# Kernel tuning notes

Hardware: AMD Instinct MI355X
Metric: run time of the kernel (lower is better)

The kernel has to match this reference:

```python
import jax, jax.numpy as jnp
import numpy as np

H = 64          # hidden_dim
TF = 24         # forecast_length


def _a_norm(N):
    # Complete graph (all i!=j) + GCNConv default self-loops => A+I = ones(N,N).
    # deg_i = N, so D^-1/2 (A+I) D^-1/2 = ones / N. Built generically below.
    A = jnp.ones((N, N), dtype=jnp.float32)
    deg = A.sum(axis=1)
    return A / jnp.sqrt(deg[:, None] * deg[None, :])


def _gcn(x, A, W, b):
    # PyG GCNConv: aggregate(norm * (x W)) + bias
    return jnp.einsum('ij,...jh->...ih', A, x @ W) + b


def setup_inputs() -> dict:
    key = jax.random.key(0)
    ks = jax.random.split(key, 20)
    B, N, T = 32, 128, 96
    s = lambda k, shape, fan: (jax.random.normal(k, shape, jnp.float32) / np.sqrt(max(fan, 1)))
    return {
        'x': jax.random.normal(ks[0], (B, N, T), jnp.float32),
        # spatial GCN stack
        'W_s1': s(ks[1], (1, H), 1), 'b_s1': jnp.zeros((H,), jnp.float32),
        'W_s2': s(ks[2], (H, H), H), 'b_s2': jnp.zeros((H,), jnp.float32),
        # temporal attention MLP
        'Wa1': s(ks[3], (H, H), H), 'ba1': jnp.zeros((H,), jnp.float32),
        'Wa2': s(ks[4], (H, 1), H), 'ba2': jnp.zeros((1,), jnp.float32),
        # GRU (single step, h0 = 0)
        'W_ih': s(ks[5], (3 * H, H), H), 'W_hh': s(ks[6], (3 * H, H), H),
        'b_ih': jnp.zeros((3 * H,), jnp.float32), 'b_hh': jnp.zeros((3 * H,), jnp.float32),
        # ODE-func GCN stack
        'W_o1': s(ks[7], (H, H), H), 'b_o1': jnp.zeros((H,), jnp.float32),
        'W_o2': s(ks[8], (H, H), H), 'b_o2': jnp.zeros((H,), jnp.float32),
        # output head
        'W_out': s(ks[9], (H, 1), H), 'b_out': jnp.zeros((1,), jnp.float32),
    }


def reference(x, W_s1, b_s1, W_s2, b_s2, Wa1, ba1, Wa2, ba2,
              W_ih, W_hh, b_ih, b_hh, W_o1, b_o1, W_o2, b_o2, W_out, b_out):
    B, N, T = x.shape
    A = _a_norm(N)

    # --- spatial encoding, vectorized over (batch, time) ---
    xt = jnp.transpose(x, (0, 2, 1))[..., None]          # (B, T, N, 1)
    h = jax.nn.relu(_gcn(xt, A, W_s1, b_s1))             # (B, T, N, H)
    h = jax.nn.relu(_gcn(h, A, W_s2, b_s2))

    # --- temporal attention over time axis ---
    att = jnp.tanh(h @ Wa1 + ba1) @ Wa2 + ba2            # (B, T, N, 1)
    w = jax.nn.softmax(att, axis=1)
    nf = jnp.sum(h * w, axis=1)                          # (B, N, H)

    # --- one-step GRU encoder with zero initial hidden ---
    gi = nf.reshape(B * N, -1) @ W_ih.T + b_ih           # (B*N, 3H)
    gi_r, gi_z, gi_n = jnp.split(gi, 3, axis=-1)
    bh_r, bh_z, bh_n = jnp.split(b_hh, 3)
    r = jax.nn.sigmoid(gi_r + bh_r)
    z = jax.nn.sigmoid(gi_z + bh_z)
    n = jnp.tanh(gi_n + r * bh_n)
    hidden = ((1.0 - z) * n).reshape(B, N, -1)           # (B, N, H)

    # --- graph ODE derivative: two GCN layers + tanh ---
    def f(y):
        y = jnp.tanh(_gcn(y, A, W_o1, b_o1))
        y = jnp.tanh(_gcn(y, A, W_o2, b_o2))
        return y

    # torchdiffeq fixed-grid 'rk4' (3/8 rule) on t = linspace(0, TF, TF)
    dt = jnp.float32(TF / (TF - 1))
    third = jnp.float32(1.0 / 3.0)

    def step(y, _):
        k1 = f(y)
        k2 = f(y + dt * k1 * third)
        k3 = f(y + dt * (k2 - k1 * third))
        k4 = f(y + dt * (k1 - k2 + k3))
        y1 = y + dt * (k1 + 3.0 * (k2 + k3) + k4) * jnp.float32(0.125)
        return y1, y1

    _, ys = jax.lax.scan(step, hidden, None, length=TF - 1)
    traj = jnp.concatenate([hidden[None], ys], axis=0)   # (TF, B, N, H)

    # output head then rearrange to (B, N, TF)
    preds = (traj @ W_out + b_out)[..., 0]               # (TF, B, N)
    return jnp.transpose(preds, (1, 2, 0))
```

## Files before the change

kernel.cpp:

```cpp
#include <hip/hip_runtime.h>


#define BN 32
#define NN 128
#define TT 96
#define HH 64
#define TFC 24

#if defined(__has_builtin)
#if __has_builtin(__builtin_amdgcn_fdot2)
#define HAVE_FDOT2 1
#endif
#if __has_builtin(__builtin_amdgcn_update_dpp)
#define HAVE_DPP 1
#endif
#endif

using half2v = __fp16 __attribute__((ext_vector_type(2)));
typedef _Float16 half8 __attribute__((ext_vector_type(8)));
typedef float f32x4 __attribute__((ext_vector_type(4)));

__device__ __forceinline__ unsigned pack_pair(float a, float b) {
    union { half2v h; unsigned u; } c;
    c.h = __builtin_amdgcn_cvt_pkrtz(a, b);
    return c.u;
}
__device__ __forceinline__ half2v as_h2(unsigned u) {
    union { unsigned u; half2v h; } c; c.u = u; return c.h;
}
__device__ __forceinline__ unsigned rdlu(unsigned v, int l) {
    return (unsigned)__builtin_amdgcn_readlane((int)v, l);
}
__device__ __forceinline__ float rdl(float v, int l) {
    return __int_as_float(__builtin_amdgcn_readlane(__float_as_int(v), l));
}

template <int CTRL>
__device__ __forceinline__ float dppf(float x) {
#if HAVE_DPP
    return __int_as_float(
        __builtin_amdgcn_update_dpp(0, __float_as_int(x), CTRL, 0xF, 0xF, true));
#else
    return 0.f;
#endif
}

__device__ __forceinline__ float xor1(float x) {
#if HAVE_DPP
    return dppf<0xB1>(x);
#else
    return __shfl_xor(x, 1, 64);
#endif
}

__device__ __forceinline__ float wave_sum(float v) {
#if HAVE_DPP
    v += dppf<0xB1>(v);
    v += dppf<0x4E>(v);
    v += dppf<0x141>(v);
    v += dppf<0x140>(v);
    return ((rdl(v, 0) + rdl(v, 16)) + (rdl(v, 32) + rdl(v, 48)));
#else
#pragma unroll
    for (int off = 32; off > 0; off >>= 1) v += __shfl_xor(v, off, 64);
    return v;
#endif
}
__device__ __forceinline__ void wave_sum2(float& a, float& b) {
#if HAVE_DPP
    a += dppf<0xB1>(a);  b += dppf<0xB1>(b);
    a += dppf<0x4E>(a);  b += dppf<0x4E>(b);
    a += dppf<0x141>(a); b += dppf<0x141>(b);
    a += dppf<0x140>(a); b += dppf<0x140>(b);
    a = (rdl(a, 0) + rdl(a, 16)) + (rdl(a, 32) + rdl(a, 48));
    b = (rdl(b, 0) + rdl(b, 16)) + (rdl(b, 32) + rdl(b, 48));
#else
    a = wave_sum(a); b = wave_sum(b);
#endif
}
__device__ __forceinline__ float wave_max(float v) {
#if HAVE_DPP
    v = fmaxf(v, dppf<0xB1>(v));
    v = fmaxf(v, dppf<0x4E>(v));
    v = fmaxf(v, dppf<0x141>(v));
    v = fmaxf(v, dppf<0x140>(v));
    return fmaxf(fmaxf(rdl(v, 0), rdl(v, 16)), fmaxf(rdl(v, 32), rdl(v, 48)));
#else
#pragma unroll
    for (int off = 32; off > 0; off >>= 1) v = fmaxf(v, __shfl_xor(v, off, 64));
    return v;
#endif
}

__device__ __forceinline__ float dot2acc(unsigned w, unsigned up, float acc) {
#if HAVE_FDOT2
    return __builtin_amdgcn_fdot2(as_h2(w), as_h2(up), acc, false);
#else
    const half2v wh = as_h2(w), uh = as_h2(up);
    return fmaf((float)wh.y, (float)uh.y, fmaf((float)wh.x, (float)uh.x, acc));
#endif
}

#define PMV64_2(WP, UA, UB, RA, RB)                                        \
    do {                                                                   \
        float a0 = 0.f, a1 = 0.f, a2 = 0.f, a3 = 0.f;                      \
        float b0 = 0.f, b1 = 0.f, b2 = 0.f, b3 = 0.f;                      \
        _Pragma("unroll")                                                  \
        for (int k = 0; k < 32; k += 4) {                                  \
            const unsigned ua0 = rdlu(UA, 2 * k);                          \
            const unsigned ub0 = rdlu(UB, 2 * k);                          \
            const unsigned ua1 = rdlu(UA, 2 * k + 2);                      \
            const unsigned ub1 = rdlu(UB, 2 * k + 2);                      \
            const unsigned ua2 = rdlu(UA, 2 * k + 4);                      \
            const unsigned ub2 = rdlu(UB, 2 * k + 4);                      \
            const unsigned ua3 = rdlu(UA, 2 * k + 6);                      \
            const unsigned ub3 = rdlu(UB, 2 * k + 6);                      \
            a0 = dot2acc(WP[k],     ua0, a0);                              \
            b0 = dot2acc(WP[k],     ub0, b0);                              \
            a1 = dot2acc(WP[k + 1], ua1, a1);                              \
            b1 = dot2acc(WP[k + 1], ub1, b1);                              \
            a2 = dot2acc(WP[k + 2], ua2, a2);                              \
            b2 = dot2acc(WP[k + 2], ub2, b2);                              \
            a3 = dot2acc(WP[k + 3], ua3, a3);                              \
            b3 = dot2acc(WP[k + 3], ub3, b3);                              \
        }                                                                  \
        RA = (a0 + a1) + (a2 + a3);                                        \
        RB = (b0 + b1) + (b2 + b3);                                        \
    } while (0)

__device__ __forceinline__ float fast_tanh(float x) {
    float e = __expf(2.f * x);
    return 1.f - 2.f * __builtin_amdgcn_rcpf(e + 1.f);
}
__device__ __forceinline__ float fast_sigmoid(float x) {
    return __builtin_amdgcn_rcpf(1.f + __expf(-x));
}

__global__ __launch_bounds__(256) void spatial_kernel(
    const float* __restrict__ x,    const float* __restrict__ Ws1,
    const float* __restrict__ bs1,  const float* __restrict__ Ws2,
    const float* __restrict__ bs2,  const float* __restrict__ Wa1,
    const float* __restrict__ ba1,  const float* __restrict__ Wa2,
    unsigned* __restrict__ ws_h2,   float* __restrict__ ws_att)
{
    const int tid  = threadIdx.x;
    const int lane = tid & 63;
    const int w    = tid >> 6;
    const int tq   = blockIdx.x;
    const int b    = blockIdx.y;
    const int tbase = tq * 24;

    __shared__ float xbar[24];
    if (tid < 24) {
        const float* xb = x + (size_t)b * NN * TT + (tbase + tid);
        float s = 0.f;
#pragma unroll
        for (int n = 0; n < NN; ++n) s += xb[n * TT];
        xbar[tid] = s * (1.f / 128.f);
    }

    const float ws1l = Ws1[lane];
    const float bs1l = bs1[lane];
    const float bs2l = bs2[lane];
    const float ba1l = ba1[lane];
    const float wa2l = Wa2[lane];
    unsigned ws2p[32], wa1p[32];
#pragma unroll
    for (int k = 0; k < 32; ++k) {
        ws2p[k] = pack_pair(Ws2[(2 * k) * HH + lane], Ws2[(2 * k + 1) * HH + lane]);
        wa1p[k] = pack_pair(Wa1[(2 * k) * HH + lane], Wa1[(2 * k + 1) * HH + lane]);
    }
#pragma unroll
    for (int k = 0; k < 32; ++k) {
        asm volatile("" : "+v"(ws2p[k]), "+v"(wa1p[k]));
    }
    __syncthreads();

#pragma unroll 1
    for (int i = 0; i < 3; ++i) {
        const int tl0 = w * 6 + 2 * i;
        const float sA = xbar[tl0];
        const float sB = xbar[tl0 + 1];
        const float h1A = fmaxf(fmaf(sA, ws1l, bs1l), 0.f);
        const float h1B = fmaxf(fmaf(sB, ws1l, bs1l), 0.f);
        const unsigned uA = pack_pair(h1A, xor1(h1A));
        const unsigned uB = pack_pair(h1B, xor1(h1B));
        float accA, accB;
        PMV64_2(ws2p, uA, uB, accA, accB);
        const float h2A = fmaxf(accA + bs2l, 0.f);
        const float h2B = fmaxf(accB + bs2l, 0.f);
        ws_h2[((size_t)b * (TT / 2) + (tbase + tl0) / 2) * HH + lane] =
            pack_pair(h2A, h2B);

        const unsigned vA = pack_pair(h2A, xor1(h2A));
        const unsigned vB = pack_pair(h2B, xor1(h2B));
        PMV64_2(wa1p, vA, vB, accA, accB);
        float gA = fast_tanh(accA + ba1l) * wa2l;
        float gB = fast_tanh(accB + ba1l) * wa2l;
        wave_sum2(gA, gB);
        if (lane == 0) {
            ws_att[b * TT + tbase + tl0]     = gA;
            ws_att[b * TT + tbase + tl0 + 1] = gB;
        }
    }
}

__global__ __launch_bounds__(64)
__attribute__((amdgpu_waves_per_eu(1, 1)))
void ode_kernel(
    const unsigned* __restrict__ ws_h2, const float* __restrict__ ws_att,
    const float* __restrict__ Wih,  const float* __restrict__ bih,
    const float* __restrict__ bhh,  const float* __restrict__ Wo1,
    const float* __restrict__ bo1p, const float* __restrict__ Wo2,
    const float* __restrict__ bo2p, const float* __restrict__ Wout,
    const float* __restrict__ boutp, float* __restrict__ out)
{
    const int lane = threadIdx.x;
    const int b    = blockIdx.x;

    const float a0s = ws_att[b * TT + lane];
    const float a1s = (lane < TT - 64) ? ws_att[b * TT + 64 + lane] : -1e30f;
    const float m = wave_max(fmaxf(a0s, a1s));
    const float e0 = __expf(a0s - m);
    const float e1 = (lane < TT - 64) ? __expf(a1s - m) : 0.f;
    const float inv = __builtin_amdgcn_rcpf(wave_sum(e0 + e1));
    const float q0 = e0 * inv;
    const float q1 = e1 * inv;

    const unsigned* h2b = ws_h2 + (size_t)b * (TT / 2) * HH;
    unsigned hp[TT / 2];
#pragma unroll
    for (int tp = 0; tp < TT / 2; ++tp) hp[tp] = h2b[tp * HH + lane];
    float nf = 0.f;
#pragma unroll
    for (int tp = 0; tp < 32; ++tp) {
        const unsigned qp = pack_pair(rdl(q0, 2 * tp), rdl(q0, 2 * tp + 1));
        nf = dot2acc(hp[tp], qp, nf);
    }
#pragma unroll
    for (int tp = 32; tp < TT / 2; ++tp) {
        const unsigned qp = pack_pair(rdl(q1, 2 * tp - 64), rdl(q1, 2 * tp - 63));
        nf = dot2acc(hp[tp], qp, nf);
    }

    float gr = bih[lane];
    float gz = bih[64 + lane];
    float gn = bih[128 + lane];
#pragma unroll
    for (int j = 0; j < HH; j += 4) {
        const float4 wr = *(const float4*)&Wih[(size_t)lane * HH + j];
        const float4 wz = *(const float4*)&Wih[(size_t)(64 + lane) * HH + j];
        const float4 wn = *(const float4*)&Wih[(size_t)(128 + lane) * HH + j];
        const float n0 = rdl(nf, j), n1 = rdl(nf, j + 1);
        const float n2 = rdl(nf, j + 2), n3 = rdl(nf, j + 3);
        gr += n0 * wr.x + n1 * wr.y + n2 * wr.z + n3 * wr.w;
        gz += n0 * wz.x + n1 * wz.y + n2 * wz.z + n3 * wz.w;
        gn += n0 * wn.x + n1 * wn.y + n2 * wn.z + n3 * wn.w;
    }
    const float r = fast_sigmoid(gr + bhh[lane]);
    const float z = fast_sigmoid(gz + bhh[64 + lane]);
    const float n = fast_tanh(gn + r * bhh[128 + lane]);
    float y = (1.f - z) * n;

    const int col16 = lane & 15;
    const int grp   = lane >> 4;
    union Frag { unsigned u4[4]; half8 h; };
    Frag B1[4][2], B2[4][2];
#pragma unroll
    for (int t = 0; t < 4; ++t) {
#pragma unroll
        for (int s = 0; s < 2; ++s) {
#pragma unroll
            for (int rr = 0; rr < 4; ++rr) {
                const int k = 32 * s + 8 * grp + 2 * rr;
                const int j = 16 * t + col16;
                B1[t][s].u4[rr] = pack_pair(Wo1[k * HH + j], Wo1[(k + 1) * HH + j]);
                B2[t][s].u4[rr] = pack_pair(Wo2[k * HH + j], Wo2[(k + 1) * HH + j]);
            }
        }
    }
#pragma unroll
    for (int t = 0; t < 4; ++t) {
#pragma unroll
        for (int s = 0; s < 2; ++s) {
            asm volatile("" : "+v"(B1[t][s].h), "+v"(B2[t][s].h));
        }
    }
    const float bo1 = bo1p[lane];
    const float bo2 = bo2p[lane];
    const float wo  = Wout[lane];
    const float bo  = boutp[0];

    const int ab0 = 32 * grp;
    const bool s1 = (grp == 1), s2 = (grp == 2), s3 = (grp == 3);
    const f32x4 CZERO = {0.f, 0.f, 0.f, 0.f};

    auto f_eval = [&](float u) -> float {
        Frag A0, A1;
        const unsigned up = pack_pair(u, xor1(u));
#pragma unroll
        for (int rr = 0; rr < 4; ++rr) {
            A0.u4[rr] = (unsigned)__builtin_amdgcn_ds_bpermute(ab0 + 8 * rr, (int)up);
            A1.u4[rr] = (unsigned)__builtin_amdgcn_ds_bpermute(ab0 + 128 + 8 * rr, (int)up);
        }
        f32x4 c0 = __builtin_amdgcn_mfma_f32_16x16x32_f16(A0.h, B1[0][0].h, CZERO, 0, 0, 0);
        f32x4 c1 = __builtin_amdgcn_mfma_f32_16x16x32_f16(A0.h, B1[1][0].h, CZERO, 0, 0, 0);
        f32x4 c2 = __builtin_amdgcn_mfma_f32_16x16x32_f16(A0.h, B1[2][0].h, CZERO, 0, 0, 0);
        f32x4 c3 = __builtin_amdgcn_mfma_f32_16x16x32_f16(A0.h, B1[3][0].h, CZERO, 0, 0, 0);
        c0 = __builtin_amdgcn_mfma_f32_16x16x32_f16(A1.h, B1[0][1].h, c0, 0, 0, 0);
        c1 = __builtin_amdgcn_mfma_f32_16x16x32_f16(A1.h, B1[1][1].h, c1, 0, 0, 0);
        c2 = __builtin_amdgcn_mfma_f32_16x16x32_f16(A1.h, B1[2][1].h, c2, 0, 0, 0);
        c3 = __builtin_amdgcn_mfma_f32_16x16x32_f16(A1.h, B1[3][1].h, c3, 0, 0, 0);
        float v = s1 ? c1[0] : c0[0];
        v = s2 ? c2[0] : v;
        v = s3 ? c3[0] : v;
        v = fast_tanh(v + bo1);
        const unsigned vp = pack_pair(v, xor1(v));
#pragma unroll
        for (int rr = 0; rr < 4; ++rr) {
            A0.u4[rr] = (unsigned)__builtin_amdgcn_ds_bpermute(ab0 + 8 * rr, (int)vp);
            A1.u4[rr] = (unsigned)__builtin_amdgcn_ds_bpermute(ab0 + 128 + 8 * rr, (int)vp);
        }
        c0 = __builtin_amdgcn_mfma_f32_16x16x32_f16(A0.h, B2[0][0].h, CZERO, 0, 0, 0);
        c1 = __builtin_amdgcn_mfma_f32_16x16x32_f16(A0.h, B2[1][0].h, CZERO, 0, 0, 0);
        c2 = __builtin_amdgcn_mfma_f32_16x16x32_f16(A0.h, B2[2][0].h, CZERO, 0, 0, 0);
        c3 = __builtin_amdgcn_mfma_f32_16x16x32_f16(A0.h, B2[3][0].h, CZERO, 0, 0, 0);
        c0 = __builtin_amdgcn_mfma_f32_16x16x32_f16(A1.h, B2[0][1].h, c0, 0, 0, 0);
        c1 = __builtin_amdgcn_mfma_f32_16x16x32_f16(A1.h, B2[1][1].h, c1, 0, 0, 0);
        c2 = __builtin_amdgcn_mfma_f32_16x16x32_f16(A1.h, B2[2][1].h, c2, 0, 0, 0);
        c3 = __builtin_amdgcn_mfma_f32_16x16x32_f16(A1.h, B2[3][1].h, c3, 0, 0, 0);
        float o = s1 ? c1[0] : c0[0];
        o = s2 ? c2[0] : o;
        o = s3 ? c3[0] : o;
        return fast_tanh(o + bo2);
    };

    float* ob = out + (size_t)b * NN * TFC;
    {
        const float p = wave_sum(y * wo) + bo;
        ob[lane * TFC]        = p;
        ob[(64 + lane) * TFC] = p;
    }

    const float dt = (float)(24.0 / 23.0);
    const float third = 1.f / 3.f;

#pragma unroll 1
    for (int st = 0; st < TFC - 1; ++st) {
        const float k1 = f_eval(y);
        const float k2 = f_eval(y + dt * k1 * third);
        const float k3 = f_eval(y + dt * (k2 - k1 * third));
        const float k4 = f_eval(y + dt * (k1 - k2 + k3));
        y = y + dt * (k1 + 3.f * (k2 + k3) + k4) * 0.125f;
        const float p = wave_sum(y * wo) + bo;
        ob[lane * TFC + st + 1]        = p;
        ob[(64 + lane) * TFC + st + 1] = p;
    }
}

extern "C" void kernel_launch(void* const* d_in, const int* in_sizes, int n_in,
                              void* d_out, int out_size, void* d_ws, size_t ws_size,
                              hipStream_t stream) {
    (void)in_sizes; (void)n_in; (void)ws_size; (void)out_size;
    const float* x    = (const float*)d_in[0];
    const float* Ws1  = (const float*)d_in[1];
    const float* bs1  = (const float*)d_in[2];
    const float* Ws2  = (const float*)d_in[3];
    const float* bs2  = (const float*)d_in[4];
    const float* Wa1  = (const float*)d_in[5];
    const float* ba1  = (const float*)d_in[6];
    const float* Wa2  = (const float*)d_in[7];
    const float* Wih  = (const float*)d_in[9];
    const float* bih  = (const float*)d_in[11];
    const float* bhh  = (const float*)d_in[12];
    const float* Wo1  = (const float*)d_in[13];
    const float* bo1  = (const float*)d_in[14];
    const float* Wo2  = (const float*)d_in[15];
    const float* bo2  = (const float*)d_in[16];
    const float* Wout = (const float*)d_in[17];
    const float* bout = (const float*)d_in[18];

    unsigned* ws_h2 = (unsigned*)d_ws;
    float* ws_att   = (float*)((char*)d_ws + (size_t)BN * (TT / 2) * HH * 4);

    spatial_kernel<<<dim3(4, BN), dim3(256), 0, stream>>>(
        x, Ws1, bs1, Ws2, bs2, Wa1, ba1, Wa2, ws_h2, ws_att);

    ode_kernel<<<dim3(BN), dim3(64), 0, stream>>>(
        ws_h2, ws_att, Wih, bih, bhh, Wo1, bo1, Wo2, bo2, Wout, bout,
        (float*)d_out);
}
```

Measured before the change: 125.5 us.

## Fuse spatial and ODE kernels into one 1024-thread block per batch

Merges the spatial encoding/attention kernel and the GRU+ODE kernel into a single kernel with one 1024-thread block per batch. Intermediate h2 and attention scores move from global workspace to shared memory, and only wave 0 continues into the sequential ODE phase after a block barrier. This removes one launch and the global round trip between stages. In exchange it removes the launch_bounds(64)/waves_per_eu hints from the ODE phase, so its register budget is now bounded by the 1024-thread launch, which may force spills in the serial RK4 loop.

```diff
diff --git a/kernel.cpp b/kernel.cpp
--- a/kernel.cpp
+++ b/kernel.cpp
@@ -136,23 +136,28 @@
     return __builtin_amdgcn_rcpf(1.f + __expf(-x));
 }
 
-__global__ __launch_bounds__(256) void spatial_kernel(
+__global__ __launch_bounds__(1024) void fused_kernel(
     const float* __restrict__ x,    const float* __restrict__ Ws1,
     const float* __restrict__ bs1,  const float* __restrict__ Ws2,
     const float* __restrict__ bs2,  const float* __restrict__ Wa1,
     const float* __restrict__ ba1,  const float* __restrict__ Wa2,
-    unsigned* __restrict__ ws_h2,   float* __restrict__ ws_att)
+    const float* __restrict__ Wih,  const float* __restrict__ bih,
+    const float* __restrict__ bhh,  const float* __restrict__ Wo1,
+    const float* __restrict__ bo1p, const float* __restrict__ Wo2,
+    const float* __restrict__ bo2p, const float* __restrict__ Wout,
+    const float* __restrict__ boutp, float* __restrict__ out)
 {
     const int tid  = threadIdx.x;
     const int lane = tid & 63;
     const int w    = tid >> 6;
-    const int tq   = blockIdx.x;
-    const int b    = blockIdx.y;
-    const int tbase = tq * 24;
-
-    __shared__ float xbar[24];
-    if (tid < 24) {
-        const float* xb = x + (size_t)b * NN * TT + (tbase + tid);
+    const int b    = blockIdx.x;
+
+    __shared__ float xbar[TT];
+    __shared__ unsigned h2s[(TT / 2) * HH];
+    __shared__ float atts[TT];
+
+    if (tid < TT) {
+        const float* xb = x + (size_t)b * NN * TT + tid;
         float s = 0.f;
 #pragma unroll
         for (int n = 0; n < NN; ++n) s += xb[n * TT];
@@ -189,8 +194,7 @@
         PMV64_2(ws2p, uA, uB, accA, accB);
         const float h2A = fmaxf(accA + bs2l, 0.f);
         const float h2B = fmaxf(accB + bs2l, 0.f);
-        ws_h2[((size_t)b * (TT / 2) + (tbase + tl0) / 2) * HH + lane] =
-            pack_pair(h2A, h2B);
+        h2s[(tl0 / 2) * HH + lane] = pack_pair(h2A, h2B);
 
         const unsigned vA = pack_pair(h2A, xor1(h2A));
         const unsigned vB = pack_pair(h2B, xor1(h2B));
@@ -199,27 +203,16 @@
         float gB = fast_tanh(accB + ba1l) * wa2l;
         wave_sum2(gA, gB);
         if (lane == 0) {
-            ws_att[b * TT + tbase + tl0]     = gA;
-            ws_att[b * TT + tbase + tl0 + 1] = gB;
-        }
-    }
-}
-
-__global__ __launch_bounds__(64)
-__attribute__((amdgpu_waves_per_eu(1, 1)))
-void ode_kernel(
-    const unsigned* __restrict__ ws_h2, const float* __restrict__ ws_att,
-    const float* __restrict__ Wih,  const float* __restrict__ bih,
-    const float* __restrict__ bhh,  const float* __restrict__ Wo1,
-    const float* __restrict__ bo1p, const float* __restrict__ Wo2,
-    const float* __restrict__ bo2p, const float* __restrict__ Wout,
-    const float* __restrict__ boutp, float* __restrict__ out)
-{
-    const int lane = threadIdx.x;
-    const int b    = blockIdx.x;
-
-    const float a0s = ws_att[b * TT + lane];
-    const float a1s = (lane < TT - 64) ? ws_att[b * TT + 64 + lane] : -1e30f;
+            atts[tl0]     = gA;
+            atts[tl0 + 1] = gB;
+        }
+    }
+    __syncthreads();
+
+    if (w != 0) return;
+
+    const float a0s = atts[lane];
+    const float a1s = (lane < TT - 64) ? atts[64 + lane] : -1e30f;
     const float m = wave_max(fmaxf(a0s, a1s));
     const float e0 = __expf(a0s - m);
     const float e1 = (lane < TT - 64) ? __expf(a1s - m) : 0.f;
@@ -227,20 +220,18 @@
     const float q0 = e0 * inv;
     const float q1 = e1 * inv;
 
-    const unsigned* h2b = ws_h2 + (size_t)b * (TT / 2) * HH;
-    unsigned hp[TT / 2];
-#pragma unroll
-    for (int tp = 0; tp < TT / 2; ++tp) hp[tp] = h2b[tp * HH + lane];
     float nf = 0.f;
 #pragma unroll
     for (int tp = 0; tp < 32; ++tp) {
+        const unsigned hpv = h2s[tp * HH + lane];
         const unsigned qp = pack_pair(rdl(q0, 2 * tp), rdl(q0, 2 * tp + 1));
-        nf = dot2acc(hp[tp], qp, nf);
+        nf = dot2acc(hpv, qp, nf);
     }
 #pragma unroll
     for (int tp = 32; tp < TT / 2; ++tp) {
+        const unsigned hpv = h2s[tp * HH + lane];
         const unsigned qp = pack_pair(rdl(q1, 2 * tp - 64), rdl(q1, 2 * tp - 63));
-        nf = dot2acc(hp[tp], qp, nf);
+        nf = dot2acc(hpv, qp, nf);
     }
 
     float gr = bih[lane];
@@ -361,7 +352,7 @@
 extern "C" void kernel_launch(void* const* d_in, const int* in_sizes, int n_in,
                               void* d_out, int out_size, void* d_ws, size_t ws_size,
                               hipStream_t stream) {
-    (void)in_sizes; (void)n_in; (void)ws_size; (void)out_size;
+    (void)in_sizes; (void)n_in; (void)ws_size; (void)out_size; (void)d_ws;
     const float* x    = (const float*)d_in[0];
     const float* Ws1  = (const float*)d_in[1];
     const float* bs1  = (const float*)d_in[2];
@@ -380,13 +371,8 @@
     const float* Wout = (const float*)d_in[17];
     const float* bout = (const float*)d_in[18];
 
-    unsigned* ws_h2 = (unsigned*)d_ws;
-    float* ws_att   = (float*)((char*)d_ws + (size_t)BN * (TT / 2) * HH * 4);
-
-    spatial_kernel<<<dim3(4, BN), dim3(256), 0, stream>>>(
-        x, Ws1, bs1, Ws2, bs2, Wa1, ba1, Wa2, ws_h2, ws_att);
-
-    ode_kernel<<<dim3(BN), dim3(64), 0, stream>>>(
-        ws_h2, ws_att, Wih, bih, bhh, Wo1, bo1, Wo2, bo2, Wout, bout,
+    fused_kernel<<<dim3(BN), dim3(1024), 0, stream>>>(
+        x, Ws1, bs1, Ws2, bs2, Wa1, ba1, Wa2,
+        Wih, bih, bhh, Wo1, bo1, Wo2, bo2, Wout, bout,
         (float*)d_out);
 }
```

Measured after the change: 131.2 us. +4.5%, slower.
